# Performance work log

Hardware: AMD Instinct MI355X
Metric: run time of the kernel (lower is better)

## Reference

```python
import jax, jax.numpy as jnp
import numpy as np

D = 256          # hidden_dim
H = 4            # num_heads
HD = D // H      # head_dim = 64
E = 4            # num_experts (hard-coded in MoE)
TOPK = 2         # top_k (hard-coded)
DFF = 2 * D      # expert ffn width
EPS = 1e-5


def _ln(x, g, b):
    mu = x.mean(-1, keepdims=True)
    var = x.var(-1, keepdims=True)  # biased, matches torch LayerNorm
    return (x - mu) * jax.lax.rsqrt(var + EPS) * g + b


def _ff(x, w1, b1, w2, b2):
    h = jax.nn.gelu(x @ w1 + b1, approximate=False)  # torch nn.GELU default = exact erf
    return h @ w2 + b2


def setup_inputs() -> dict:
    key = jax.random.key(0)
    ks = jax.random.split(key, 24)
    B, S, IN = 4, 2048, 256
    s = 0.02
    inp = {
        'x': jax.random.normal(ks[0], (B, S, IN), jnp.float32),
        'mask': jax.random.randint(ks[1], (B, S), 0, 2).astype(jnp.int32),
        'w_in': jax.random.normal(ks[2], (IN, D), jnp.float32) * s,
        'b_in': jnp.zeros((D,), jnp.float32),
        'g1': jnp.ones((D,), jnp.float32),
        'be1': jnp.zeros((D,), jnp.float32),
        'wq': jax.random.normal(ks[3], (D, D), jnp.float32) * s,
        'bq': jnp.zeros((D,), jnp.float32),
        'wk': jax.random.normal(ks[4], (D, D), jnp.float32) * s,
        'bk': jnp.zeros((D,), jnp.float32),
        'wv': jax.random.normal(ks[5], (D, D), jnp.float32) * s,
        'bv': jnp.zeros((D,), jnp.float32),
        'wo': jax.random.normal(ks[6], (D, D), jnp.float32) * s,
        'bo': jnp.zeros((D,), jnp.float32),
        'g2': jnp.ones((D,), jnp.float32),
        'be2': jnp.zeros((D,), jnp.float32),
        'wg': jax.random.normal(ks[7], (D, E), jnp.float32) * s,
        'bg': jnp.zeros((E,), jnp.float32),
        'ew1': jax.random.normal(ks[8], (E, D, DFF), jnp.float32) * s,
        'eb1': jnp.zeros((E, DFF), jnp.float32),
        'ew2': jax.random.normal(ks[9], (E, DFF, D), jnp.float32) * s,
        'eb2': jnp.zeros((E, D), jnp.float32),
    }
    return inp


def reference(x, mask, w_in, b_in, g1, be1, wq, bq, wk, bk, wv, bv, wo, bo, g2, be2, wg, bg, ew1, eb1, ew2, eb2):
    B, S, _ = x.shape
    x = x @ w_in + b_in
    res = x
    h = _ln(x, g1, be1)
    q = (h @ wq + bq).reshape(B, S, H, HD).transpose(0, 2, 1, 3)  # bhsd
    k = (h @ wk + bk).reshape(B, S, H, HD).transpose(0, 2, 1, 3)
    v = (h @ wv + bv).reshape(B, S, H, HD).transpose(0, 2, 1, 3)
    # RoPE (interleaved pairs, half-concat output, as in source)
    inv_freq = 1.0 / (10000.0 ** (jnp.arange(0, HD, 2, dtype=jnp.float32) / HD))
    ang = jnp.arange(S, dtype=jnp.float32)[:, None] * inv_freq[None, :]  # [S, HD//2]
    sin, cos = jnp.sin(ang), jnp.cos(ang)  # broadcast over (B,H)
    def rot(t):
        ts = t.reshape(B, H, S, HD // 2, 2)
        t0, t1 = ts[..., 0], ts[..., 1]
        return jnp.concatenate([t0 * cos - t1 * sin, t1 * cos + t0 * sin], axis=-1)
    qr, kr = rot(q), rot(k)
    attn = jnp.einsum('bhqd,bhkd->bhqk', qr, kr) * (HD ** -0.5)
    row = mask[:, None, :, None]  # [B,1,S,1] -> masks whole query rows
    attn = jnp.where(row == 0, jnp.float32(-1e4), attn)
    valid = (row * S).astype(jnp.float32)           # [B,1,S,1]
    all_masked = valid == 0
    uniform = jnp.where(row != 0, 1.0 / jnp.maximum(valid, 1.0), 0.0)
    attn = jnp.where(all_masked, uniform, attn)
    attn = jax.nn.softmax(attn, axis=-1)
    out = jnp.einsum('bhqk,bhkd->bhqd', attn, v).transpose(0, 2, 1, 3).reshape(B, S, D)
    out = out @ wo + bo
    x = res + out
    res2 = x
    h2 = _ln(x, g2, be2)
    # MoE (faithful: expert i only applied where top-k slot i picked expert i)
    gp = jax.nn.softmax(h2 @ wg + bg, axis=-1)
    topv, topi = jax.lax.top_k(gp, TOPK)
    moe_out = jnp.zeros_like(h2)
    for i in range(TOPK):
        eo = _ff(h2, ew1[i], eb1[i], ew2[i], eb2[i])
        m = (topi[..., i] == i)[..., None].astype(h2.dtype)
        moe_out = moe_out + m * eo * topv[..., i:i + 1]
    flat = topi.reshape(-1)
    total = sum((flat == i).sum() for i in range(TOPK)).astype(jnp.float32)
    usage = jnp.zeros((E,), jnp.float32) + total
    usage = usage / usage.sum()
    lb = (jnp.std(usage, ddof=1) / usage.mean()) ** 2
    y = res2 + h2  # source discards moe_out / lb (likely a bug); kept live with exact 0* add
    return y + 0.0 * (moe_out.sum() + lb)
```

## Files before the change

### kernel.cpp

```cpp
#include <hip/hip_runtime.h>
#include <cstddef>

#define Bb    4
#define Sq    2048
#define Dd    256
#define Hh    4
#define HDh   64
#define NROWS (Bb*Sq)
#define EPSf  1e-5f

typedef unsigned short u16;
typedef unsigned int   u32;
typedef unsigned long long u64;
typedef __attribute__((ext_vector_type(8))) short  frag_ab;
typedef __attribute__((ext_vector_type(4))) float  frag_cd;

__device__ __forceinline__ u16 f2bf(float f){
    union { float f; u32 u; } v; v.f = f;
    u32 r = v.u + 0x7fffu + ((v.u >> 16) & 1u);
    return (u16)(r >> 16);
}
__device__ __forceinline__ u16 f2bf_trunc(float f){
    union { float f; u32 u; } v; v.f = f;
    return (u16)(v.u >> 16);
}
__device__ __forceinline__ float bf2f(u32 u){
    union { u32 u; float f; } v; v.u = u << 16; return v.f;
}

__global__ __launch_bounds__(256) void k0_prep(
    const float* __restrict__ w_in, const float* __restrict__ wq,
    const float* __restrict__ wk,   const float* __restrict__ wv,
    const float* __restrict__ wo,
    u16* __restrict__ wT, float* __restrict__ tab)
{
    const int bid = blockIdx.x, tid = threadIdx.x;
    if (bid < 80){
        __shared__ float T[64][65];
        const int wsel = bid >> 4, tile = bid & 15;
        const int k0 = (tile >> 2) * 64, n0 = (tile & 3) * 64;
        const float* src = wsel==0 ? w_in : wsel==1 ? wq : wsel==2 ? wk
                         : wsel==3 ? wv : wo;
        #pragma unroll
        for (int i=0;i<16;++i){
            int idx = i*256 + tid, k = idx>>6, n = idx&63;
            T[k][n] = src[(size_t)(k0+k)*Dd + n0 + n];
        }
        __syncthreads();
        u16* dst = wT + (size_t)wsel*Dd*Dd;
        #pragma unroll
        for (int i=0;i<16;++i){
            int idx = i*256 + tid, n = idx>>6, k = idx&63;
            dst[(size_t)(n0+n)*Dd + k0 + k] = f2bf(T[k][n]);
        }
    } else {
        int s = (bid-80)*8 + (tid>>5);
        int p = tid & 31;
        float invf = exp2f(-(float)p * (13.287712379549449f/32.f));
        float sn, cs; sincosf((float)s * invf, &sn, &cs);
        tab[(size_t)s*64 + p]      = cs;
        tab[(size_t)s*64 + 32 + p] = sn;
    }
}

__global__ __launch_bounds__(256) void k1_fused(
    const float* __restrict__ x,  const float* __restrict__ tab,
    const u16* __restrict__ wTin, const u16* __restrict__ wTq,
    const u16* __restrict__ wTk,  const u16* __restrict__ wTv,
    const float* __restrict__ b_in, const float* __restrict__ g1,
    const float* __restrict__ be1,  const float* __restrict__ bq,
    const float* __restrict__ bk,   const float* __restrict__ bv,
    float* __restrict__ x1, u16* __restrict__ qro,
    u16* __restrict__ kro,  u16* __restrict__ vto)
{
    const int tid  = threadIdx.x;
    const int w    = tid >> 6;
    const int lane = tid & 63;
    const int l16  = lane & 15;
    const int quad = lane >> 4;
    const int r0   = blockIdx.x * 16;
    const int b    = r0 >> 11;
    const int s0   = r0 & (Sq-1);
    const int cb   = w * 64;

    __shared__ u16 Xs[16][264];
    __shared__ u16 Hs[16][264];
    __shared__ u16 Os[16][264];
    __shared__ float red[2][16][4];

    #pragma unroll
    for (int i=0;i<4;++i){
        int f = i*256 + tid;
        int row = f>>6, c4 = f&63;
        float4 v4 = *(const float4*)(x + (size_t)(r0+row)*Dd + c4*4);
        u16 pk4[4] = { f2bf(v4.x), f2bf(v4.y), f2bf(v4.z), f2bf(v4.w) };
        *(u64*)&Xs[row][c4*4] = *(u64*)pk4;
    }
    __syncthreads();

    float bin4[4], g4[4], be4[4];
    #pragma unroll
    for (int nt=0;nt<4;++nt){
        int col = cb + nt*16 + l16;
        bin4[nt] = b_in[col]; g4[nt] = g1[col]; be4[nt] = be1[col];
    }

    frag_cd acc[4];
    #pragma unroll
    for (int nt=0;nt<4;++nt) acc[nt] = (frag_cd){bin4[nt],bin4[nt],bin4[nt],bin4[nt]};
    #pragma unroll
    for (int kc=0;kc<8;++kc){
        frag_ab a = *(frag_ab*)&Xs[l16][kc*32 + quad*8];
        #pragma unroll
        for (int nt=0;nt<4;++nt){
            frag_ab bf = *(const frag_ab*)&wTin[(size_t)(cb+nt*16+l16)*Dd + kc*32 + quad*8];
            acc[nt] = __builtin_amdgcn_mfma_f32_16x16x32_bf16(a, bf, acc[nt], 0,0,0);
        }
    }

    #pragma unroll
    for (int r=0;r<4;++r){
        float s=0.f, q=0.f;
        #pragma unroll
        for (int nt=0;nt<4;++nt){
            float v = acc[nt][r];
            x1[(size_t)(r0+quad*4+r)*Dd + cb + nt*16 + l16] = v;
            s += v; q += v*v;
        }
        s += __shfl_xor(s,1); q += __shfl_xor(q,1);
        s += __shfl_xor(s,2); q += __shfl_xor(q,2);
        s += __shfl_xor(s,4); q += __shfl_xor(q,4);
        s += __shfl_xor(s,8); q += __shfl_xor(q,8);
        if (l16==0){ red[0][quad*4+r][w]=s; red[1][quad*4+r][w]=q; }
    }
    __syncthreads();

    #pragma unroll
    for (int r=0;r<4;++r){
        int row = quad*4 + r;
        float mu = (red[0][row][0]+red[0][row][1]+red[0][row][2]+red[0][row][3])*(1.f/Dd);
        float ms = (red[1][row][0]+red[1][row][1]+red[1][row][2]+red[1][row][3])*(1.f/Dd);
        float rstd = rsqrtf(ms - mu*mu + EPSf);
        #pragma unroll
        for (int nt=0;nt<4;++nt){
            float hv = (acc[nt][r]-mu)*rstd*g4[nt] + be4[nt];
            Hs[row][cb + nt*16 + l16] = f2bf(hv);
        }
    }
    __syncthreads();

    const u16*   wps[3] = { wTq, wTk, wTv };
    const float* bps[3] = { bq, bk, bv };
    #pragma unroll
    for (int tt=0; tt<3; ++tt){
        frag_cd a2[4];
        #pragma unroll
        for (int nt=0;nt<4;++nt){
            float bb = bps[tt][cb + nt*16 + l16];
            a2[nt] = (frag_cd){bb,bb,bb,bb};
        }
        #pragma unroll
        for (int kc=0;kc<8;++kc){
            frag_ab a = *(frag_ab*)&Hs[l16][kc*32 + quad*8];
            #pragma unroll
            for (int nt=0;nt<4;++nt){
                frag_ab bf = *(const frag_ab*)&wps[tt][(size_t)(cb+nt*16+l16)*Dd + kc*32 + quad*8];
                a2[nt] = __builtin_amdgcn_mfma_f32_16x16x32_bf16(a, bf, a2[nt], 0,0,0);
            }
        }
        #pragma unroll
        for (int r=0;r<4;++r)
            #pragma unroll
            for (int nt=0;nt<4;++nt)
                Os[quad*4+r][cb + nt*16 + l16] = f2bf(a2[nt][r]);
        __syncthreads();

        if (tt < 2){
            const int row  = tid >> 4;
            const int head = (tid >> 2) & 3;
            const int pq   = tid & 3;
            const int s    = s0 + row;
            const float* tb = tab + (size_t)s*64;
            float4 c0 = *(const float4*)(tb + pq*8);
            float4 c1 = *(const float4*)(tb + pq*8 + 4);
            float4 sn0 = *(const float4*)(tb + 32 + pq*8);
            float4 sn1 = *(const float4*)(tb + 32 + pq*8 + 4);
            const float cA[8] = {c0.x,c0.y,c0.z,c0.w,c1.x,c1.y,c1.z,c1.w};
            const float sA[8] = {sn0.x,sn0.y,sn0.z,sn0.w,sn1.x,sn1.y,sn1.z,sn1.w};
            u16* dst = (tt==0 ? qro : kro) + ((size_t)(b*Hh+head)*Sq + s)*HDh;
            u16 lo[8], hi[8];
            #pragma unroll
            for (int j=0;j<8;++j){
                int p = pq*8 + j;
                u32 pr = *(const u32*)&Os[row][head*64 + 2*p];
                float t0 = bf2f(pr & 0xffffu), t1 = bf2f(pr >> 16);
                lo[j] = f2bf(t0*cA[j] - t1*sA[j]);
                hi[j] = f2bf(t1*cA[j] + t0*sA[j]);
            }
            *(float4*)(dst + pq*8)      = *(float4*)lo;
            *(float4*)(dst + 32 + pq*8) = *(float4*)hi;
        } else {
            const int head = tid >> 6, d = tid & 63;
            u16 pk[16];
            #pragma unroll
            for (int j=0;j<16;++j) pk[j] = Os[j][head*64 + d];
            u16* dst = vto + ((size_t)(b*Hh+head)*HDh + d)*Sq + s0;
            *(float4*)dst     = *(float4*)pk;
            *(float4*)(dst+8) = *(float4*)&pk[8];
        }
        __syncthreads();
    }
}

__global__ __launch_bounds__(256) void k2_attn(
    const u16* __restrict__ qr, const u16* __restrict__ kr,
    const u16* __restrict__ vt, const int* __restrict__ mask,
    float* __restrict__ Opart, float* __restrict__ lpart)
{
    const int tid = threadIdx.x;
    const int w   = tid >> 6;
    const int lane= tid & 63;
    const int l16 = lane & 15;
    const int quad= lane >> 4;
    const int qt  = blockIdx.x;
    const int bh  = blockIdx.y;
    const int ks  = blockIdx.z;
    const int b   = bh >> 2;
    const int q0  = qt * 64;

    __shared__ u16 Qs [64][72];
    __shared__ u16 Ks [64][72];
    __shared__ u16 Vts[64][72];
    __shared__ u16 Ps [4][16][72];

    const u16* qg = qr + ((size_t)bh*Sq + q0)*HDh;
    for (int cc=tid; cc<512; cc+=256){
        int row = cc>>3, part = cc&7;
        *(float4*)&Qs[row][part*8] = *(const float4*)(qg + row*HDh + part*8);
    }
    __syncthreads();

    frag_ab qf0 = *(frag_ab*)&Qs[w*16 + l16][quad*8];
    frag_ab qf1 = *(frag_ab*)&Qs[w*16 + l16][quad*8 + 32];

    float mf2[4];
    #pragma unroll
    for (int r=0;r<4;++r)
        mf2[r] = (mask[(size_t)b*Sq + q0 + w*16 + quad*4 + r] != 0)
               ? 0.125f*1.44269504f : 0.f;

    float lrow[4];
    #pragma unroll
    for (int r=0;r<4;++r) lrow[r] = 0.f;
    frag_cd O[4];
    #pragma unroll
    for (int d=0; d<4; ++d) O[d] = (frag_cd){0.f,0.f,0.f,0.f};

    const u16* kg0 = kr + (size_t)bh*Sq*HDh + (size_t)ks*1024*HDh;
    const u16* vg0 = vt + (size_t)bh*HDh*Sq + (size_t)ks*1024;

    for (int kt=0; kt<16; ++kt){
        __syncthreads();
        const u16* kg = kg0 + (size_t)kt*64*HDh;
        const u16* vg = vg0 + kt*64;
        for (int cc=tid; cc<512; cc+=256){
            int row = cc>>3, part = cc&7;
            *(float4*)&Ks[row][part*8]  = *(const float4*)(kg + row*HDh  + part*8);
            *(float4*)&Vts[row][part*8] = *(const float4*)(vg + (size_t)row*Sq + part*8);
        }
        __syncthreads();

        frag_cd sc[4];
        #pragma unroll
        for (int t=0;t<4;++t){
            frag_ab kf0 = *(frag_ab*)&Ks[t*16 + l16][quad*8];
            frag_ab kf1 = *(frag_ab*)&Ks[t*16 + l16][quad*8 + 32];
            frag_cd z = (frag_cd){0.f,0.f,0.f,0.f};
            z = __builtin_amdgcn_mfma_f32_16x16x32_bf16(qf0, kf0, z, 0,0,0);
            z = __builtin_amdgcn_mfma_f32_16x16x32_bf16(qf1, kf1, z, 0,0,0);
            sc[t] = z;
        }

        #pragma unroll
        for (int t=0;t<4;++t)
            #pragma unroll
            for (int r=0;r<4;++r){
                float p = exp2f(sc[t][r]*mf2[r]);
                lrow[r] += p;
                Ps[w][quad*4+r][t*16 + l16] = f2bf_trunc(p);
            }

        frag_ab pf0 = *(frag_ab*)&Ps[w][l16][quad*8];
        frag_ab pf1 = *(frag_ab*)&Ps[w][l16][quad*8 + 32];

        #pragma unroll
        for (int d=0; d<4; ++d){
            frag_ab vf0 = *(frag_ab*)&Vts[d*16 + l16][quad*8];
            frag_ab vf1 = *(frag_ab*)&Vts[d*16 + l16][quad*8 + 32];
            O[d] = __builtin_amdgcn_mfma_f32_16x16x32_bf16(pf0, vf0, O[d], 0,0,0);
            O[d] = __builtin_amdgcn_mfma_f32_16x16x32_bf16(pf1, vf1, O[d], 0,0,0);
        }
    }

    float* Ob = Opart + (((size_t)ks*16 + bh)*Sq)*HDh;
    #pragma unroll
    for (int r=0;r<4;++r){
        size_t ro = (size_t)(q0 + w*16 + quad*4 + r)*HDh + l16;
        #pragma unroll
        for (int d=0; d<4; ++d)
            Ob[ro + d*16] = O[d][r];
        float s = lrow[r];
        s += __shfl_xor(s,1);
        s += __shfl_xor(s,2);
        s += __shfl_xor(s,4);
        s += __shfl_xor(s,8);
        if (l16 == 0)
            lpart[((size_t)ks*16 + bh)*Sq + q0 + w*16 + quad*4 + r] = s;
    }
}

__global__ __launch_bounds__(256) void k3_gemm_ln(
    const float* __restrict__ Opart, const float* __restrict__ lpart,
    const u16* __restrict__ wTo,
    const float* __restrict__ bo, const float* __restrict__ x1,
    const float* __restrict__ g2, const float* __restrict__ be2,
    float* __restrict__ out)
{
    const int tid  = threadIdx.x;
    const int w    = tid >> 6;
    const int lane = tid & 63;
    const int l16  = lane & 15;
    const int quad = lane >> 4;
    const int r0   = blockIdx.x * 16;
    const int b    = r0 >> 11;
    const int s0   = r0 & (Sq-1);
    const int cb   = w * 64;

    __shared__ u16 Ats[16][264];
    __shared__ float red[2][16][4];
    __shared__ float linv[4][16];

    if (tid < 64){
        int h = tid >> 4, r = tid & 15;
        size_t li = ((size_t)(b*Hh + h))*Sq + s0 + r;
        linv[h][r] = 1.f / (lpart[li] + lpart[(size_t)16*Sq + li]);
    }
    __syncthreads();

    const size_t SPLIT = (size_t)16*Sq*HDh;
    #pragma unroll
    for (int i=0;i<4;++i){
        int idx = i*256 + tid;
        int h = idx >> 8, rem = idx & 255, row = rem >> 4, c = rem & 15;
        size_t base = (((size_t)(b*Hh + h))*Sq + s0 + row)*HDh + c*4;
        float4 o0 = *(const float4*)(Opart + base);
        float4 o1 = *(const float4*)(Opart + SPLIT + base);
        float li = linv[h][row];
        u16 pk[4] = { f2bf((o0.x+o1.x)*li), f2bf((o0.y+o1.y)*li),
                      f2bf((o0.z+o1.z)*li), f2bf((o0.w+o1.w)*li) };
        *(u64*)&Ats[row][h*64 + c*4] = *(u64*)pk;
    }
    __syncthreads();

    float g4[4], be4[4];
    frag_cd acc[4];
    #pragma unroll
    for (int nt=0;nt<4;++nt){
        int col = cb + nt*16 + l16;
        float bb = bo[col];
        acc[nt] = (frag_cd){bb,bb,bb,bb};
        g4[nt] = g2[col]; be4[nt] = be2[col];
    }
    #pragma unroll
    for (int kc=0;kc<8;++kc){
        frag_ab a = *(frag_ab*)&Ats[l16][kc*32 + quad*8];
        #pragma unroll
        for (int nt=0;nt<4;++nt){
            frag_ab bf = *(const frag_ab*)&wTo[(size_t)(cb+nt*16+l16)*Dd + kc*32 + quad*8];
            acc[nt] = __builtin_amdgcn_mfma_f32_16x16x32_bf16(a, bf, acc[nt], 0,0,0);
        }
    }

    #pragma unroll
    for (int r=0;r<4;++r){
        float s=0.f, q=0.f;
        #pragma unroll
        for (int nt=0;nt<4;++nt){
            float v = acc[nt][r] + x1[(size_t)(r0+quad*4+r)*Dd + cb + nt*16 + l16];
            acc[nt][r] = v;
            s += v; q += v*v;
        }
        s += __shfl_xor(s,1); q += __shfl_xor(q,1);
        s += __shfl_xor(s,2); q += __shfl_xor(q,2);
        s += __shfl_xor(s,4); q += __shfl_xor(q,4);
        s += __shfl_xor(s,8); q += __shfl_xor(q,8);
        if (l16==0){ red[0][quad*4+r][w]=s; red[1][quad*4+r][w]=q; }
    }
    __syncthreads();

    #pragma unroll
    for (int r=0;r<4;++r){
        int row = quad*4 + r;
        float mu = (red[0][row][0]+red[0][row][1]+red[0][row][2]+red[0][row][3])*(1.f/Dd);
        float ms = (red[1][row][0]+red[1][row][1]+red[1][row][2]+red[1][row][3])*(1.f/Dd);
        float rstd = rsqrtf(ms - mu*mu + EPSf);
        #pragma unroll
        for (int nt=0;nt<4;++nt){
            float v = acc[nt][r];
            float h2 = (v-mu)*rstd*g4[nt] + be4[nt];
            out[(size_t)(r0+row)*Dd + cb + nt*16 + l16] = v + h2;
        }
    }
}

extern "C" void kernel_launch(void* const* d_in, const int* in_sizes, int n_in,
                              void* d_out, int out_size, void* d_ws, size_t ws_size,
                              hipStream_t stream)
{
    const float* x    = (const float*)d_in[0];
    const int*   mask = (const int*)  d_in[1];
    const float* w_in = (const float*)d_in[2];
    const float* b_in = (const float*)d_in[3];
    const float* g1   = (const float*)d_in[4];
    const float* be1  = (const float*)d_in[5];
    const float* wq   = (const float*)d_in[6];
    const float* bq   = (const float*)d_in[7];
    const float* wk   = (const float*)d_in[8];
    const float* bk   = (const float*)d_in[9];
    const float* wv   = (const float*)d_in[10];
    const float* bv   = (const float*)d_in[11];
    const float* wo   = (const float*)d_in[12];
    const float* bo   = (const float*)d_in[13];
    const float* g2   = (const float*)d_in[14];
    const float* be2  = (const float*)d_in[15];

    float* out = (float*)d_out;
    char*  wsb = (char*)d_ws;

    float* x1    = (float*)(wsb);
    float* tab   = (float*)(wsb + ( 8u<<20));
    u16*   qro   = (u16*)(wsb + (12u<<20));
    u16*   kro   = (u16*)(wsb + (16u<<20));
    u16*   vto   = (u16*)(wsb + (20u<<20));
    float* Opart = (float*)(wsb + (24u<<20));
    float* lpart = (float*)(wsb + (40u<<20));
    u16*   wT    = (u16*)(wsb + (40u<<20) + (512u<<10));

    k0_prep<<<336, 256, 0, stream>>>(w_in, wq, wk, wv, wo, wT, tab);
    k1_fused<<<NROWS/16, 256, 0, stream>>>(
        x, tab, wT, wT + Dd*Dd, wT + 2*Dd*Dd, wT + 3*Dd*Dd,
        b_in, g1, be1, bq, bk, bv, x1, qro, kro, vto);
    k2_attn<<<dim3(Sq/64, Bb*Hh, 2), 256, 0, stream>>>(qro, kro, vto, mask, Opart, lpart);
    k3_gemm_ln<<<NROWS/16, 256, 0, stream>>>(Opart, lpart, wT + 4*Dd*Dd,
                                             bo, x1, g2, be2, out);
}
```

Baseline: 189.8 us.

## Preload weight fragments into registers, prefetch K/V tiles, store attention partials as bf16

The QKV/input and output-projection GEMMs now load all B-fragments for a weight matrix into registers up front, and fetch the next weight set early so the loads overlap other work. Launch bounds are set to 2 blocks per SM. The attention kernel prefetches the next K/V tile into registers while computing on the current one. Split-K attention partial outputs are stored in bf16 instead of fp32, which halves that traffic at some cost in precision. The large register arrays (bfr[8][4]) risk spills or lower occupancy.

Result: slower. 227.4 us (+19.8%).

```diff
diff --git a/kernel.cpp b/kernel.cpp
--- a/kernel.cpp
+++ b/kernel.cpp
@@ -63,7 +63,7 @@
     }
 }
 
-__global__ __launch_bounds__(256) void k1_fused(
+__global__ __launch_bounds__(256,2) void k1_fused(
     const float* __restrict__ x,  const float* __restrict__ tab,
     const u16* __restrict__ wTin, const u16* __restrict__ wTq,
     const u16* __restrict__ wTk,  const u16* __restrict__ wTv,
@@ -88,6 +88,15 @@
     __shared__ u16 Os[16][264];
     __shared__ float red[2][16][4];
 
+    const size_t woff = (size_t)(cb + l16)*Dd + quad*8;
+    frag_ab bfr[8][4];
+
+    #pragma unroll
+    for (int kc=0;kc<8;++kc)
+        #pragma unroll
+        for (int nt=0;nt<4;++nt)
+            bfr[kc][nt] = *(const frag_ab*)&wTin[woff + (size_t)nt*16*Dd + kc*32];
+
     #pragma unroll
     for (int i=0;i<4;++i){
         int f = i*256 + tid;
@@ -112,11 +121,15 @@
     for (int kc=0;kc<8;++kc){
         frag_ab a = *(frag_ab*)&Xs[l16][kc*32 + quad*8];
         #pragma unroll
-        for (int nt=0;nt<4;++nt){
-            frag_ab bf = *(const frag_ab*)&wTin[(size_t)(cb+nt*16+l16)*Dd + kc*32 + quad*8];
-            acc[nt] = __builtin_amdgcn_mfma_f32_16x16x32_bf16(a, bf, acc[nt], 0,0,0);
-        }
-    }
+        for (int nt=0;nt<4;++nt)
+            acc[nt] = __builtin_amdgcn_mfma_f32_16x16x32_bf16(a, bfr[kc][nt], acc[nt], 0,0,0);
+    }
+
+    #pragma unroll
+    for (int kc=0;kc<8;++kc)
+        #pragma unroll
+        for (int nt=0;nt<4;++nt)
+            bfr[kc][nt] = *(const frag_ab*)&wTq[woff + (size_t)nt*16*Dd + kc*32];
 
     #pragma unroll
     for (int r=0;r<4;++r){
@@ -149,7 +162,6 @@
     }
     __syncthreads();
 
-    const u16*   wps[3] = { wTq, wTk, wTv };
     const float* bps[3] = { bq, bk, bv };
     #pragma unroll
     for (int tt=0; tt<3; ++tt){
@@ -163,10 +175,21 @@
         for (int kc=0;kc<8;++kc){
             frag_ab a = *(frag_ab*)&Hs[l16][kc*32 + quad*8];
             #pragma unroll
-            for (int nt=0;nt<4;++nt){
-                frag_ab bf = *(const frag_ab*)&wps[tt][(size_t)(cb+nt*16+l16)*Dd + kc*32 + quad*8];
-                a2[nt] = __builtin_amdgcn_mfma_f32_16x16x32_bf16(a, bf, a2[nt], 0,0,0);
-            }
+            for (int nt=0;nt<4;++nt)
+                a2[nt] = __builtin_amdgcn_mfma_f32_16x16x32_bf16(a, bfr[kc][nt], a2[nt], 0,0,0);
+        }
+        if (tt==0){
+            #pragma unroll
+            for (int kc=0;kc<8;++kc)
+                #pragma unroll
+                for (int nt=0;nt<4;++nt)
+                    bfr[kc][nt] = *(const frag_ab*)&wTk[woff + (size_t)nt*16*Dd + kc*32];
+        } else if (tt==1){
+            #pragma unroll
+            for (int kc=0;kc<8;++kc)
+                #pragma unroll
+                for (int nt=0;nt<4;++nt)
+                    bfr[kc][nt] = *(const frag_ab*)&wTv[woff + (size_t)nt*16*Dd + kc*32];
         }
         #pragma unroll
         for (int r=0;r<4;++r)
@@ -215,7 +238,7 @@
 __global__ __launch_bounds__(256) void k2_attn(
     const u16* __restrict__ qr, const u16* __restrict__ kr,
     const u16* __restrict__ vt, const int* __restrict__ mask,
-    float* __restrict__ Opart, float* __restrict__ lpart)
+    u16* __restrict__ Opart, float* __restrict__ lpart)
 {
     const int tid = threadIdx.x;
     const int w   = tid >> 6;
@@ -259,16 +282,30 @@
     const u16* kg0 = kr + (size_t)bh*Sq*HDh + (size_t)ks*1024*HDh;
     const u16* vg0 = vt + (size_t)bh*HDh*Sq + (size_t)ks*1024;
 
+    const int srow = tid>>3, spart = tid&7;
+    const int srow2 = (tid+256)>>3;
+    float4 kpre[2], vpre[2];
+    kpre[0] = *(const float4*)(kg0 + srow*HDh  + spart*8);
+    kpre[1] = *(const float4*)(kg0 + srow2*HDh + spart*8);
+    vpre[0] = *(const float4*)(vg0 + (size_t)srow*Sq  + spart*8);
+    vpre[1] = *(const float4*)(vg0 + (size_t)srow2*Sq + spart*8);
+
     for (int kt=0; kt<16; ++kt){
         __syncthreads();
-        const u16* kg = kg0 + (size_t)kt*64*HDh;
-        const u16* vg = vg0 + kt*64;
-        for (int cc=tid; cc<512; cc+=256){
-            int row = cc>>3, part = cc&7;
-            *(float4*)&Ks[row][part*8]  = *(const float4*)(kg + row*HDh  + part*8);
-            *(float4*)&Vts[row][part*8] = *(const float4*)(vg + (size_t)row*Sq + part*8);
-        }
+        *(float4*)&Ks [srow ][spart*8] = kpre[0];
+        *(float4*)&Ks [srow2][spart*8] = kpre[1];
+        *(float4*)&Vts[srow ][spart*8] = vpre[0];
+        *(float4*)&Vts[srow2][spart*8] = vpre[1];
         __syncthreads();
+
+        if (kt < 15){
+            const u16* kg = kg0 + (size_t)(kt+1)*64*HDh;
+            const u16* vg = vg0 + (kt+1)*64;
+            kpre[0] = *(const float4*)(kg + srow*HDh  + spart*8);
+            kpre[1] = *(const float4*)(kg + srow2*HDh + spart*8);
+            vpre[0] = *(const float4*)(vg + (size_t)srow*Sq  + spart*8);
+            vpre[1] = *(const float4*)(vg + (size_t)srow2*Sq + spart*8);
+        }
 
         frag_cd sc[4];
         #pragma unroll
@@ -302,13 +339,13 @@
         }
     }
 
-    float* Ob = Opart + (((size_t)ks*16 + bh)*Sq)*HDh;
+    u16* Ob = Opart + (((size_t)ks*16 + bh)*Sq)*HDh;
     #pragma unroll
     for (int r=0;r<4;++r){
         size_t ro = (size_t)(q0 + w*16 + quad*4 + r)*HDh + l16;
         #pragma unroll
         for (int d=0; d<4; ++d)
-            Ob[ro + d*16] = O[d][r];
+            Ob[ro + d*16] = f2bf(O[d][r]);
         float s = lrow[r];
         s += __shfl_xor(s,1);
         s += __shfl_xor(s,2);
@@ -319,8 +356,8 @@
     }
 }
 
-__global__ __launch_bounds__(256) void k3_gemm_ln(
-    const float* __restrict__ Opart, const float* __restrict__ lpart,
+__global__ __launch_bounds__(256,2) void k3_gemm_ln(
+    const u16* __restrict__ Opart, const float* __restrict__ lpart,
     const u16* __restrict__ wTo,
     const float* __restrict__ bo, const float* __restrict__ x1,
     const float* __restrict__ g2, const float* __restrict__ be2,
@@ -340,6 +377,21 @@
     __shared__ float red[2][16][4];
     __shared__ float linv[4][16];
 
+    const size_t woff = (size_t)(cb + l16)*Dd + quad*8;
+    frag_ab bfr[8][4];
+    #pragma unroll
+    for (int kc=0;kc<8;++kc)
+        #pragma unroll
+        for (int nt=0;nt<4;++nt)
+            bfr[kc][nt] = *(const frag_ab*)&wTo[woff + (size_t)nt*16*Dd + kc*32];
+
+    float x1v[4][4];
+    #pragma unroll
+    for (int r=0;r<4;++r)
+        #pragma unroll
+        for (int nt=0;nt<4;++nt)
+            x1v[r][nt] = x1[(size_t)(r0+quad*4+r)*Dd + cb + nt*16 + l16];
+
     if (tid < 64){
         int h = tid >> 4, r = tid & 15;
         size_t li = ((size_t)(b*Hh + h))*Sq + s0 + r;
@@ -353,11 +405,16 @@
         int idx = i*256 + tid;
         int h = idx >> 8, rem = idx & 255, row = rem >> 4, c = rem & 15;
         size_t base = (((size_t)(b*Hh + h))*Sq + s0 + row)*HDh + c*4;
-        float4 o0 = *(const float4*)(Opart + base);
-        float4 o1 = *(const float4*)(Opart + SPLIT + base);
+        u64 p0 = *(const u64*)(Opart + base);
+        u64 p1 = *(const u64*)(Opart + SPLIT + base);
         float li = linv[h][row];
-        u16 pk[4] = { f2bf((o0.x+o1.x)*li), f2bf((o0.y+o1.y)*li),
-                      f2bf((o0.z+o1.z)*li), f2bf((o0.w+o1.w)*li) };
+        u16 pk[4];
+        #pragma unroll
+        for (int j=0;j<4;++j){
+            float v0 = bf2f((u32)((p0 >> (16*j)) & 0xffffu));
+            float v1 = bf2f((u32)((p1 >> (16*j)) & 0xffffu));
+            pk[j] = f2bf((v0+v1)*li);
+        }
         *(u64*)&Ats[row][h*64 + c*4] = *(u64*)pk;
     }
     __syncthreads();
@@ -375,10 +432,8 @@
     for (int kc=0;kc<8;++kc){
         frag_ab a = *(frag_ab*)&Ats[l16][kc*32 + quad*8];
         #pragma unroll
-        for (int nt=0;nt<4;++nt){
-            frag_ab bf = *(const frag_ab*)&wTo[(size_t)(cb+nt*16+l16)*Dd + kc*32 + quad*8];
-            acc[nt] = __builtin_amdgcn_mfma_f32_16x16x32_bf16(a, bf, acc[nt], 0,0,0);
-        }
+        for (int nt=0;nt<4;++nt)
+            acc[nt] = __builtin_amdgcn_mfma_f32_16x16x32_bf16(a, bfr[kc][nt], acc[nt], 0,0,0);
     }
 
     #pragma unroll
@@ -386,7 +441,7 @@
         float s=0.f, q=0.f;
         #pragma unroll
         for (int nt=0;nt<4;++nt){
-            float v = acc[nt][r] + x1[(size_t)(r0+quad*4+r)*Dd + cb + nt*16 + l16];
+            float v = acc[nt][r] + x1v[r][nt];
             acc[nt][r] = v;
             s += v; q += v*v;
         }
@@ -442,9 +497,9 @@
     u16*   qro   = (u16*)(wsb + (12u<<20));
     u16*   kro   = (u16*)(wsb + (16u<<20));
     u16*   vto   = (u16*)(wsb + (20u<<20));
-    float* Opart = (float*)(wsb + (24u<<20));
-    float* lpart = (float*)(wsb + (40u<<20));
-    u16*   wT    = (u16*)(wsb + (40u<<20) + (512u<<10));
+    u16*   Opart = (u16*)(wsb + (24u<<20));
+    float* lpart = (float*)(wsb + (32u<<20));
+    u16*   wT    = (u16*)(wsb + (33u<<20));
 
     k0_prep<<<336, 256, 0, stream>>>(w_in, wq, wk, wv, wo, wT, tab);
     k1_fused<<<NROWS/16, 256, 0, stream>>>(
```
